# Kernel optimization log

Hardware: AMD Instinct MI355X
Metric: run time of the kernel (lower is better)

Reference implementation:

```python
import jax, jax.numpy as jnp
import numpy as np
from jax import lax

K_SIZE = 5  # dilated_kernel_size


def dcls_kernel(w, p, k=K_SIZE):
    """Build dense (Cout,Cin,k,k) kernel from DCLS v1 bilinear interpolation.
    w: (Cout,Cin,Kc) weights; p: (2,Cout,Cin,Kc) learnable positions."""
    lim = k // 2
    pos = jnp.clip(p, -lim, lim) + lim          # in [0, k-1]
    i = jnp.floor(pos).astype(jnp.int32)
    r = pos - i                                  # bilinear fractions
    Co, Ci, Kc = w.shape
    co = jnp.arange(Co)[:, None, None]
    ci = jnp.arange(Ci)[None, :, None]
    i1, i2 = i[0], i[1]
    r1, r2 = r[0], r[1]
    # scatter into (k+1)x(k+1) grid so i+1 never goes out of bounds, then trim
    K = jnp.zeros((Co, Ci, k + 1, k + 1), w.dtype)
    K = K.at[co, ci, i1,     i2    ].add(w * (1 - r1) * (1 - r2))
    K = K.at[co, ci, i1 + 1, i2    ].add(w * r1 * (1 - r2))
    K = K.at[co, ci, i1,     i2 + 1].add(w * (1 - r1) * r2)
    K = K.at[co, ci, i1 + 1, i2 + 1].add(w * r1 * r2)
    return K[:, :, :k, :k]


def conv2d(x, K, pad):
    return lax.conv_general_dilated(
        x, K, window_strides=(1, 1), padding=[(pad, pad), (pad, pad)],
        dimension_numbers=('NCHW', 'OIHW', 'NCHW'))


def maxpool2(x):
    return lax.reduce_window(x, -jnp.inf, lax.max, (1, 1, 2, 2), (1, 1, 2, 2), 'VALID')


def setup_inputs() -> dict:
    key = jax.random.key(0)
    ks = jax.random.split(key, 12)
    lim = K_SIZE // 2
    B = 4096
    x = jax.random.normal(ks[0], (B, 1, 28, 28), jnp.float32)
    w1 = jax.random.normal(ks[1], (32, 1, 16), jnp.float32) * 0.2
    p1 = jax.random.uniform(ks[2], (2, 32, 1, 16), jnp.float32, -lim, lim)
    b1 = jnp.zeros((32,), jnp.float32)
    w2 = jax.random.normal(ks[3], (64, 32, 32), jnp.float32) * 0.05
    p2 = jax.random.uniform(ks[4], (2, 64, 32, 32), jnp.float32, -lim, lim)
    b2 = jnp.zeros((64,), jnp.float32)
    fc1_w = jax.random.normal(ks[5], (128, 64 * 7 * 7), jnp.float32) * 0.02
    fc1_b = jnp.zeros((128,), jnp.float32)
    fc2_w = jax.random.normal(ks[6], (10, 128), jnp.float32) * 0.08
    fc2_b = jnp.zeros((10,), jnp.float32)
    return dict(x=x, w1=w1, p1=p1, b1=b1, w2=w2, p2=p2, b2=b2,
                fc1_w=fc1_w, fc1_b=fc1_b, fc2_w=fc2_w, fc2_b=fc2_b)


def reference(x, w1, p1, b1, w2, p2, b2, fc1_w, fc1_b, fc2_w, fc2_b):
    h = conv2d(x, dcls_kernel(w1, p1), pad=2) + b1[None, :, None, None]
    h = maxpool2(jax.nn.relu(h))                       # (B,32,14,14)
    h = conv2d(h, dcls_kernel(w2, p2), pad=2) + b2[None, :, None, None]
    h = maxpool2(jax.nn.relu(h))                       # (B,64,7,7)
    h = h.reshape(-1, 64 * 7 * 7)
    h = jax.nn.relu(h @ fc1_w.T + fc1_b)
    return h @ fc2_w.T + fc2_b                         # (B,10)
```

## Files before the change

### kernel.cpp

```cpp
#include <hip/hip_runtime.h>
#include <hip/hip_bf16.h>

typedef __attribute__((ext_vector_type(8))) short short8;
typedef __attribute__((ext_vector_type(4))) short short4v;
typedef __attribute__((ext_vector_type(4))) float float4v;

static __device__ __forceinline__ unsigned short f2bf(float f) {
    unsigned u = __float_as_uint(f);
    unsigned r = (u + 0x7FFF + ((u >> 16) & 1)) >> 16;
    return (unsigned short)r;
}

__global__ __launch_bounds__(256) void prep_all(
    const float* __restrict__ w1, const float* __restrict__ p1,
    const float* __restrict__ w2, const float* __restrict__ p2,
    const float* __restrict__ fc1w,
    unsigned short* __restrict__ K1b,
    unsigned short* __restrict__ Kt,
    unsigned short* __restrict__ w1b) {
    const int blk = blockIdx.x;
    const int t = threadIdx.x;

    if (blk < 8) {
        int cell = blk * 256 + t;
        int co = cell >> 6;
        int k = cell & 63;
        int wr = k >> 3;
        int kx = k & 7;
        float acc = 0.f;
        if (wr < 5 && kx < 5) {
#pragma unroll 8
            for (int kc = 0; kc < 16; ++kc) {
                float wv = w1[co * 16 + kc];
                float pa = p1[co * 16 + kc];
                float pb = p1[512 + co * 16 + kc];
                float pos1 = fminf(fmaxf(pa, -2.f), 2.f) + 2.f;
                float pos2 = fminf(fmaxf(pb, -2.f), 2.f) + 2.f;
                int i1 = (int)floorf(pos1);
                int i2 = (int)floorf(pos2);
                float r1 = pos1 - (float)i1;
                float r2 = pos2 - (float)i2;
                float c = 0.f;
                if (i1 == wr && i2 == kx) c += (1.f - r1) * (1.f - r2);
                if (i1 + 1 == wr && i2 == kx) c += r1 * (1.f - r2);
                if (i1 == wr && i2 + 1 == kx) c += (1.f - r1) * r2;
                if (i1 + 1 == wr && i2 + 1 == kx) c += r1 * r2;
                acc += wv * c;
            }
        }
        K1b[cell] = f2bf(acc);
    } else if (blk < 208) {
        int cell = (blk - 8) * 256 + t;
        int kk = cell >> 11;
        int co = (cell >> 5) & 63;
        int ci = cell & 31;
        int ky = kk / 5;
        int kx = kk - 5 * ky;
        const int base = (co * 32 + ci) * 32;
        float acc = 0.f;
#pragma unroll 8
        for (int kc = 0; kc < 32; ++kc) {
            float wv = w2[base + kc];
            float pa = p2[base + kc];
            float pb = p2[65536 + base + kc];
            float pos1 = fminf(fmaxf(pa, -2.f), 2.f) + 2.f;
            float pos2 = fminf(fmaxf(pb, -2.f), 2.f) + 2.f;
            int i1 = (int)floorf(pos1);
            int i2 = (int)floorf(pos2);
            float r1 = pos1 - (float)i1;
            float r2 = pos2 - (float)i2;
            float c = 0.f;
            if (i1 == ky && i2 == kx) c += (1.f - r1) * (1.f - r2);
            if (i1 + 1 == ky && i2 == kx) c += r1 * (1.f - r2);
            if (i1 == ky && i2 + 1 == kx) c += (1.f - r1) * r2;
            if (i1 + 1 == ky && i2 + 1 == kx) c += r1 * r2;
            acc += wv * c;
        }
        Kt[cell] = f2bf(acc);
    } else {
        int i8 = ((blk - 208) * 256 + t) * 8;
        float4 v0 = *(const float4*)(fc1w + i8);
        float4 v1 = *(const float4*)(fc1w + i8 + 4);
        short8 o = {(short)f2bf(v0.x), (short)f2bf(v0.y), (short)f2bf(v0.z),
                    (short)f2bf(v0.w), (short)f2bf(v1.x), (short)f2bf(v1.y),
                    (short)f2bf(v1.z), (short)f2bf(v1.w)};
        *(short8*)(w1b + i8) = o;
    }
}

__global__ __launch_bounds__(256, 4) void fused_conv_mfma(
    const float* __restrict__ x,
    const unsigned short* __restrict__ K1b,
    const unsigned short* __restrict__ Kt,
    const float* __restrict__ b1,
    const float* __restrict__ b2,
    unsigned short* __restrict__ h2) {
    __shared__ __align__(16) unsigned short h1p[18 * 20 * 40];
    __shared__ __align__(16) unsigned short sm4[4 * 29 * 44];
    __shared__ __align__(16) unsigned short sm_xb[784];

    const int b = blockIdx.x;
    const int tid = threadIdx.x;
    const int lane = tid & 63;
    const int wv = tid >> 6;
    const int n16 = lane & 15;
    const int cig = lane >> 4;

    const int yi = 2 * (n16 >> 3) + ((n16 >> 1) & 1);
    const int xi = 2 * ((n16 >> 2) & 1) + (n16 & 1);
    const int pYo = cig >> 1, pXo = cig & 1;

    for (int t = tid; t < 1800; t += 256) ((uint4*)h1p)[t] = uint4{0, 0, 0, 0};
    {
        const float* xb = x + (size_t)b * 784;
        for (int t = tid; t < 784; t += 256) sm_xb[t] = f2bf(xb[t]);
    }
    __syncthreads();

    if (tid < 116) {
        int s = tid / 29;
        int r = tid - s * 29;
        unsigned short* dst = sm4 + (s * 29 + r) * 44;
        bool rok = r < 28;
#pragma unroll
        for (int g = 0; g < 11; ++g) {
            short4v v;
#pragma unroll
            for (int e = 0; e < 4; ++e) {
                int c = g * 4 + e + s - 4;
                v[e] = (short)((rok && (unsigned)c < 28u) ? sm_xb[r * 28 + c]
                                                          : (unsigned short)0);
            }
            *(short4v*)(dst + g * 4) = v;
        }
    }

    short8 bw[2][2];
    float bias1[2], bias2[4];
#pragma unroll
    for (int cot = 0; cot < 2; ++cot) {
#pragma unroll
        for (int h = 0; h < 2; ++h)
            bw[cot][h] = *(const short8*)(K1b + (cot * 16 + n16) * 64 + h * 32 + cig * 8);
        bias1[cot] = b1[cot * 16 + n16];
    }
#pragma unroll
    for (int cot = 0; cot < 4; ++cot) bias2[cot] = b2[cot * 16 + n16];

    const int s1 = (xi + 2) & 3;
    const int pb1 = (xi + 2) & ~3;
    const unsigned short* a1base = sm4 + s1 * (29 * 44) + pb1;

    __syncthreads();

    for (int i = 0; i < 13; ++i) {
        int t = wv + 4 * i;
        if (t < 49) {
            int tY = t / 7, tX = t - 7 * tY;
            const unsigned short* ab = a1base + 4 * tX;
            int r0 = 4 * tY + yi - 2 + cig;
            int r1 = r0 + 4;
            int rr0 = ((unsigned)r0 < 28u) ? r0 : 28;
            int rr1 = ((unsigned)r1 < 28u) ? r1 : 28;
            short4v lo0 = *(const short4v*)(ab + rr0 * 44);
            short4v hi0 = *(const short4v*)(ab + rr0 * 44 + 4);
            short4v lo1 = *(const short4v*)(ab + rr1 * 44);
            short4v hi1 = *(const short4v*)(ab + rr1 * 44 + 4);
            short8 af0 = {lo0[0], lo0[1], lo0[2], lo0[3], hi0[0], hi0[1], hi0[2], hi0[3]};
            short8 af1 = {lo1[0], lo1[1], lo1[2], lo1[3], hi1[0], hi1[1], hi1[2], hi1[3]};
            int pY = 2 * tY + pYo, pX = 2 * tX + pXo;
#pragma unroll
            for (int cot = 0; cot < 2; ++cot) {
                float4v acc = {0.f, 0.f, 0.f, 0.f};
                acc = __builtin_amdgcn_mfma_f32_16x16x32_bf16(af0, bw[cot][0], acc, 0, 0, 0);
                acc = __builtin_amdgcn_mfma_f32_16x16x32_bf16(af1, bw[cot][1], acc, 0, 0, 0);
                float v = fmaxf(fmaxf(acc[0], acc[1]), fmaxf(acc[2], acc[3]));
                v = fmaxf(v + bias1[cot], 0.f);
                h1p[((pY + 2) * 20 + (pX + 2)) * 40 + cot * 16 + n16] = f2bf(v);
            }
        }
    }
    __syncthreads();

    const unsigned short* Ab[4];
    int pY2[4], pX2[4];
#pragma unroll
    for (int i = 0; i < 4; ++i) {
        int t = wv * 4 + i;
        int tY = t >> 2, tX = t & 3;
        int y2 = 4 * tY + yi;
        y2 = (y2 > 13) ? 13 : y2;
        int x2 = 4 * tX + xi;
        Ab[i] = h1p + (y2 * 20 + x2) * 40 + cig * 8;
        pY2[i] = 2 * tY + pYo;
        pX2[i] = 2 * tX + pXo;
    }

    float4v acc[4][4];
#pragma unroll
    for (int i = 0; i < 4; ++i)
#pragma unroll
        for (int c = 0; c < 4; ++c) acc[i][c] = float4v{0.f, 0.f, 0.f, 0.f};

#pragma unroll
    for (int ky = 0; ky < 5; ++ky) {
#pragma unroll
        for (int kx = 0; kx < 5; ++kx) {
            int kk = ky * 5 + kx;
            short8 wf[4];
#pragma unroll
            for (int cot = 0; cot < 4; ++cot)
                wf[cot] = *(const short8*)(Kt + ((kk * 64 + cot * 16 + n16) * 32 + cig * 8));
#pragma unroll
            for (int i = 0; i < 4; ++i) {
                short8 af = *(const short8*)(Ab[i] + (ky * 20 + kx) * 40);
#pragma unroll
                for (int cot = 0; cot < 4; ++cot)
                    acc[i][cot] = __builtin_amdgcn_mfma_f32_16x16x32_bf16(
                        af, wf[cot], acc[i][cot], 0, 0, 0);
            }
        }
    }

    unsigned short* outb = h2 + (size_t)b * 3136;
#pragma unroll
    for (int i = 0; i < 4; ++i) {
        bool ok = (pY2[i] < 7) & (pX2[i] < 7);
#pragma unroll
        for (int cot = 0; cot < 4; ++cot) {
            float4v a = acc[i][cot];
            float v = fmaxf(fmaxf(a[0], a[1]), fmaxf(a[2], a[3]));
            v = fmaxf(v + bias2[cot], 0.f);
            if (ok)
                outb[(cot * 16 + n16) * 49 + pY2[i] * 7 + pX2[i]] = f2bf(v);
        }
    }
}

__global__ __launch_bounds__(256) void fc1_mfma(
    const unsigned short* __restrict__ A,
    const unsigned short* __restrict__ Wb,
    float* __restrict__ part, size_t PB) {
    __shared__ __align__(16) unsigned short As[64 * 72];
    const int blk = blockIdx.x;
    const int kh = blk % 7;
    const int m0 = (blk / 7) * 64;
    const int tid = threadIdx.x;
    const int wv = tid >> 6;
    const int lane = tid & 63;
    const int n16 = lane & 15;
    const int cig = lane >> 4;

    float4v acc[4][2];
#pragma unroll
    for (int mt = 0; mt < 4; ++mt)
#pragma unroll
        for (int j = 0; j < 2; ++j) acc[mt][j] = float4v{0.f, 0.f, 0.f, 0.f};

    for (int it = 0; it < 7; ++it) {
        int k0 = kh * 448 + it * 64;
        __syncthreads();
#pragma unroll
        for (int i = 0; i < 2; ++i) {
            int p = tid + 256 * i;
            int r = p >> 3, ko = (p & 7) * 8;
            *(short8*)(As + r * 72 + ko) =
                *(const short8*)(A + (size_t)(m0 + r) * 3136 + k0 + ko);
        }
        __syncthreads();
#pragma unroll
        for (int h = 0; h < 2; ++h) {
            short8 af[4];
#pragma unroll
            for (int mt = 0; mt < 4; ++mt)
                af[mt] = *(const short8*)(As + (mt * 16 + n16) * 72 + h * 32 + cig * 8);
            short8 wf[2];
#pragma unroll
            for (int j = 0; j < 2; ++j)
                wf[j] = *(const short8*)(Wb + (size_t)((wv * 2 + j) * 16 + n16) * 3136 +
                                         k0 + h * 32 + cig * 8);
#pragma unroll
            for (int mt = 0; mt < 4; ++mt)
#pragma unroll
                for (int j = 0; j < 2; ++j)
                    acc[mt][j] = __builtin_amdgcn_mfma_f32_16x16x32_bf16(
                        af[mt], wf[j], acc[mt][j], 0, 0, 0);
        }
    }
    float* o = part + (size_t)kh * PB;
#pragma unroll
    for (int mt = 0; mt < 4; ++mt)
#pragma unroll
        for (int j = 0; j < 2; ++j)
#pragma unroll
            for (int r = 0; r < 4; ++r) {
                int row = m0 + mt * 16 + cig * 4 + r;
                o[(size_t)row * 128 + (wv * 2 + j) * 16 + n16] = acc[mt][j][r];
            }
}

__global__ __launch_bounds__(256) void fc2_kernel(
    const float* __restrict__ part, size_t PB,
    const float* __restrict__ fc1b,
    const float* __restrict__ W, const float* __restrict__ bias,
    float* __restrict__ out, int total4) {
    __shared__ float smW[10 * 132];
    __shared__ float smB1[128];
    __shared__ float smB[10];
    int t = threadIdx.x;
    for (int i = t; i < 1280; i += 256) {
        int n = i >> 7, k = i & 127;
        smW[n * 132 + k] = W[i];
    }
    if (t < 128) smB1[t] = fc1b[t];
    if (t < 10) smB[t] = bias[t];
    __syncthreads();
    int idx = blockIdx.x * 256 + t;
    if (idx < total4) {
        int j = idx >> 2;
        int q = idx & 3;
        int b = j / 10;
        int n = j - b * 10;
        const float* pb = part + (size_t)b * 128 + q * 32;
        const float4* bb = (const float4*)(smB1 + q * 32);
        const float4* wr = (const float4*)(smW + n * 132 + q * 32);
        float acc = 0.f;
#pragma unroll
        for (int c = 0; c < 8; ++c) {
            float4 s = *(const float4*)(pb + 4 * c);
#pragma unroll
            for (int jj = 1; jj < 7; ++jj) {
                float4 pj = *(const float4*)(pb + (size_t)jj * PB + 4 * c);
                s.x += pj.x; s.y += pj.y; s.z += pj.z; s.w += pj.w;
            }
            float4 bv = bb[c];
            float4 w = wr[c];
            acc += fmaxf(s.x + bv.x, 0.f) * w.x + fmaxf(s.y + bv.y, 0.f) * w.y +
                   fmaxf(s.z + bv.z, 0.f) * w.z + fmaxf(s.w + bv.w, 0.f) * w.w;
        }
        acc += __shfl_xor(acc, 1);
        acc += __shfl_xor(acc, 2);
        if (q == 0) out[j] = acc + smB[n];
    }
}

extern "C" void kernel_launch(void* const* d_in, const int* in_sizes, int n_in,
                              void* d_out, int out_size, void* d_ws, size_t ws_size,
                              hipStream_t stream) {
    const float* x    = (const float*)d_in[0];
    const float* w1   = (const float*)d_in[1];
    const float* p1   = (const float*)d_in[2];
    const float* b1   = (const float*)d_in[3];
    const float* w2   = (const float*)d_in[4];
    const float* p2   = (const float*)d_in[5];
    const float* b2   = (const float*)d_in[6];
    const float* fc1w = (const float*)d_in[7];
    const float* fc1b = (const float*)d_in[8];
    const float* fc2w = (const float*)d_in[9];
    const float* fc2b = (const float*)d_in[10];
    float* out = (float*)d_out;

    const int B = in_sizes[0] / 784;

    float* ws = (float*)d_ws;
    unsigned short* Kt  = (unsigned short*)ws;
    unsigned short* K1b = (unsigned short*)(ws + 25600);
    unsigned short* w1b = (unsigned short*)(ws + 26624);
    unsigned short* h2b = (unsigned short*)(ws + 227328);
    float* fc1p = ws + 227328 + (size_t)B * 1568;

    prep_all<<<404, 256, 0, stream>>>(w1, p1, w2, p2, fc1w, K1b, Kt, w1b);
    fused_conv_mfma<<<B, 256, 0, stream>>>(x, K1b, Kt, b1, b2, h2b);
    fc1_mfma<<<(B / 64) * 7, 256, 0, stream>>>(h2b, w1b, fc1p, (size_t)B * 128);
    fc2_kernel<<<(B * 10 * 4 + 255) / 256, 256, 0, stream>>>(
        fc1p, (size_t)B * 128, fc1b, fc2w, fc2b, out, B * 10 * 4);
}
```

Measured before the change: 243.4 us.

## Use 32x32x16 MFMA for conv2 and compute all fc2 outputs per row group

The conv2 stage switches from 16x16x32 bf16 MFMA tiles to 32x32x16 tiles, with a new lane-to-pixel mapping and a pooled epilogue taken from the 16-wide accumulator. The goal is fewer MFMA issues and fewer weight fragment loads per output. fc2 is restructured so each 8-lane group handles one batch row and all 10 outputs. The 7 fc1 partial sums are then reduced once per row rather than once per output. The larger accumulators raise register pressure, and the fc2 grid now assumes B is divisible by 32.

```diff
diff --git a/kernel.cpp b/kernel.cpp
--- a/kernel.cpp
+++ b/kernel.cpp
@@ -4,6 +4,7 @@
 typedef __attribute__((ext_vector_type(8))) short short8;
 typedef __attribute__((ext_vector_type(4))) short short4v;
 typedef __attribute__((ext_vector_type(4))) float float4v;
+typedef __attribute__((ext_vector_type(16))) float float16v;
 
 static __device__ __forceinline__ unsigned short f2bf(float f) {
     unsigned u = __float_as_uint(f);
@@ -110,6 +111,12 @@
     const int xi = 2 * ((n16 >> 2) & 1) + (n16 & 1);
     const int pYo = cig >> 1, pXo = cig & 1;
 
+    const int mq = lane & 31;
+    const int Qx = mq >> 2;
+    const int dy2 = (mq >> 1) & 1;
+    const int dx2 = mq & 1;
+    const int hh = lane >> 5;
+
     for (int t = tid; t < 1800; t += 256) ((uint4*)h1p)[t] = uint4{0, 0, 0, 0};
     {
         const float* xb = x + (size_t)b * 784;
@@ -136,7 +143,7 @@
     }
 
     short8 bw[2][2];
-    float bias1[2], bias2[4];
+    float bias1[2], bias2n[2];
 #pragma unroll
     for (int cot = 0; cot < 2; ++cot) {
 #pragma unroll
@@ -145,7 +152,7 @@
         bias1[cot] = b1[cot * 16 + n16];
     }
 #pragma unroll
-    for (int cot = 0; cot < 4; ++cot) bias2[cot] = b2[cot * 16 + n16];
+    for (int nt = 0; nt < 2; ++nt) bias2n[nt] = b2[nt * 32 + mq];
 
     const int s1 = (xi + 2) & 3;
     const int pb1 = (xi + 2) & ~3;
@@ -182,57 +189,72 @@
     }
     __syncthreads();
 
-    const unsigned short* Ab[4];
-    int pY2[4], pX2[4];
-#pragma unroll
-    for (int i = 0; i < 4; ++i) {
-        int t = wv * 4 + i;
-        int tY = t >> 2, tX = t & 3;
-        int y2 = 4 * tY + yi;
-        y2 = (y2 > 13) ? 13 : y2;
-        int x2 = 4 * tX + xi;
-        Ab[i] = h1p + (y2 * 20 + x2) * 40 + cig * 8;
-        pY2[i] = 2 * tY + pYo;
-        pX2[i] = 2 * tX + pXo;
-    }
-
-    float4v acc[4][4];
-#pragma unroll
-    for (int i = 0; i < 4; ++i)
-#pragma unroll
-        for (int c = 0; c < 4; ++c) acc[i][c] = float4v{0.f, 0.f, 0.f, 0.f};
+    int x2 = 2 * Qx + dx2;
+    if (x2 > 13) x2 = 13;
+    int aoff[2][2];
+    int pYv[2];
+#pragma unroll
+    for (int mt = 0; mt < 2; ++mt) {
+        int pY = 2 * wv + mt;
+        int y2 = 2 * pY + dy2;
+        if (y2 > 13) y2 = 13;
+        pYv[mt] = pY;
+#pragma unroll
+        for (int kh2 = 0; kh2 < 2; ++kh2)
+            aoff[mt][kh2] = (y2 * 20 + x2) * 40 + kh2 * 16 + hh * 8;
+    }
+
+    float16v acc2[2][2];
+#pragma unroll
+    for (int mt = 0; mt < 2; ++mt)
+#pragma unroll
+        for (int nt = 0; nt < 2; ++nt)
+#pragma unroll
+            for (int e = 0; e < 16; ++e) acc2[mt][nt][e] = 0.f;
 
 #pragma unroll
     for (int ky = 0; ky < 5; ++ky) {
 #pragma unroll
         for (int kx = 0; kx < 5; ++kx) {
             int kk = ky * 5 + kx;
-            short8 wf[4];
-#pragma unroll
-            for (int cot = 0; cot < 4; ++cot)
-                wf[cot] = *(const short8*)(Kt + ((kk * 64 + cot * 16 + n16) * 32 + cig * 8));
-#pragma unroll
-            for (int i = 0; i < 4; ++i) {
-                short8 af = *(const short8*)(Ab[i] + (ky * 20 + kx) * 40);
-#pragma unroll
-                for (int cot = 0; cot < 4; ++cot)
-                    acc[i][cot] = __builtin_amdgcn_mfma_f32_16x16x32_bf16(
-                        af, wf[cot], acc[i][cot], 0, 0, 0);
+            short8 wf[2][2];
+#pragma unroll
+            for (int nt = 0; nt < 2; ++nt)
+#pragma unroll
+                for (int kh2 = 0; kh2 < 2; ++kh2)
+                    wf[nt][kh2] = *(const short8*)(Kt + kk * 2048 +
+                        (nt * 32 + mq) * 32 + kh2 * 16 + hh * 8);
+#pragma unroll
+            for (int mt = 0; mt < 2; ++mt) {
+                short8 af0 = *(const short8*)(h1p + aoff[mt][0] + (ky * 20 + kx) * 40);
+                short8 af1 = *(const short8*)(h1p + aoff[mt][1] + (ky * 20 + kx) * 40);
+#pragma unroll
+                for (int nt = 0; nt < 2; ++nt) {
+                    acc2[mt][nt] = __builtin_amdgcn_mfma_f32_32x32x16_bf16(
+                        af0, wf[nt][0], acc2[mt][nt], 0, 0, 0);
+                    acc2[mt][nt] = __builtin_amdgcn_mfma_f32_32x32x16_bf16(
+                        af1, wf[nt][1], acc2[mt][nt], 0, 0, 0);
+                }
             }
         }
     }
 
     unsigned short* outb = h2 + (size_t)b * 3136;
 #pragma unroll
-    for (int i = 0; i < 4; ++i) {
-        bool ok = (pY2[i] < 7) & (pX2[i] < 7);
-#pragma unroll
-        for (int cot = 0; cot < 4; ++cot) {
-            float4v a = acc[i][cot];
-            float v = fmaxf(fmaxf(a[0], a[1]), fmaxf(a[2], a[3]));
-            v = fmaxf(v + bias2[cot], 0.f);
-            if (ok)
-                outb[(cot * 16 + n16) * 49 + pY2[i] * 7 + pX2[i]] = f2bf(v);
+    for (int mt = 0; mt < 2; ++mt) {
+        if (pYv[mt] < 7) {
+#pragma unroll
+            for (int nt = 0; nt < 2; ++nt) {
+#pragma unroll
+                for (int g = 0; g < 4; ++g) {
+                    int pX = 2 * g + hh;
+                    float v = fmaxf(fmaxf(acc2[mt][nt][4 * g], acc2[mt][nt][4 * g + 1]),
+                                    fmaxf(acc2[mt][nt][4 * g + 2], acc2[mt][nt][4 * g + 3]));
+                    v = fmaxf(v + bias2n[nt], 0.f);
+                    if (pX < 7)
+                        outb[(nt * 32 + mq) * 49 + pYv[mt] * 7 + pX] = f2bf(v);
+                }
+            }
         }
     }
 }
@@ -303,7 +325,7 @@
     const float* __restrict__ part, size_t PB,
     const float* __restrict__ fc1b,
     const float* __restrict__ W, const float* __restrict__ bias,
-    float* __restrict__ out, int total4) {
+    float* __restrict__ out) {
     __shared__ float smW[10 * 132];
     __shared__ float smB1[128];
     __shared__ float smB[10];
@@ -315,32 +337,48 @@
     if (t < 128) smB1[t] = fc1b[t];
     if (t < 10) smB[t] = bias[t];
     __syncthreads();
-    int idx = blockIdx.x * 256 + t;
-    if (idx < total4) {
-        int j = idx >> 2;
-        int q = idx & 3;
-        int b = j / 10;
-        int n = j - b * 10;
-        const float* pb = part + (size_t)b * 128 + q * 32;
-        const float4* bb = (const float4*)(smB1 + q * 32);
-        const float4* wr = (const float4*)(smW + n * 132 + q * 32);
-        float acc = 0.f;
-#pragma unroll
-        for (int c = 0; c < 8; ++c) {
-            float4 s = *(const float4*)(pb + 4 * c);
-#pragma unroll
-            for (int jj = 1; jj < 7; ++jj) {
-                float4 pj = *(const float4*)(pb + (size_t)jj * PB + 4 * c);
-                s.x += pj.x; s.y += pj.y; s.z += pj.z; s.w += pj.w;
-            }
-            float4 bv = bb[c];
+    const int r = t >> 3;
+    const int q = t & 7;
+    const size_t b = (size_t)blockIdx.x * 32 + r;
+    const float* pb = part + b * 128 + q * 16;
+
+    float rv[16];
+#pragma unroll
+    for (int c = 0; c < 4; ++c) {
+        float4 s = *(const float4*)(pb + 4 * c);
+#pragma unroll
+        for (int j = 1; j < 7; ++j) {
+            float4 pj = *(const float4*)(pb + (size_t)j * PB + 4 * c);
+            s.x += pj.x; s.y += pj.y; s.z += pj.z; s.w += pj.w;
+        }
+        float4 bv = *(const float4*)(smB1 + q * 16 + 4 * c);
+        rv[4 * c + 0] = fmaxf(s.x + bv.x, 0.f);
+        rv[4 * c + 1] = fmaxf(s.y + bv.y, 0.f);
+        rv[4 * c + 2] = fmaxf(s.z + bv.z, 0.f);
+        rv[4 * c + 3] = fmaxf(s.w + bv.w, 0.f);
+    }
+    float acc[10];
+#pragma unroll
+    for (int n = 0; n < 10; ++n) {
+        const float4* wr = (const float4*)(smW + n * 132 + q * 16);
+        float a = 0.f;
+#pragma unroll
+        for (int c = 0; c < 4; ++c) {
             float4 w = wr[c];
-            acc += fmaxf(s.x + bv.x, 0.f) * w.x + fmaxf(s.y + bv.y, 0.f) * w.y +
-                   fmaxf(s.z + bv.z, 0.f) * w.z + fmaxf(s.w + bv.w, 0.f) * w.w;
-        }
-        acc += __shfl_xor(acc, 1);
-        acc += __shfl_xor(acc, 2);
-        if (q == 0) out[j] = acc + smB[n];
+            a += rv[4 * c] * w.x + rv[4 * c + 1] * w.y +
+                 rv[4 * c + 2] * w.z + rv[4 * c + 3] * w.w;
+        }
+        acc[n] = a;
+    }
+#pragma unroll
+    for (int n = 0; n < 10; ++n) {
+        acc[n] += __shfl_xor(acc[n], 1);
+        acc[n] += __shfl_xor(acc[n], 2);
+        acc[n] += __shfl_xor(acc[n], 4);
+    }
+    if (q == 0) {
+#pragma unroll
+        for (int n = 0; n < 10; ++n) out[b * 10 + n] = acc[n] + smB[n];
     }
 }
 
@@ -372,6 +410,6 @@
     prep_all<<<404, 256, 0, stream>>>(w1, p1, w2, p2, fc1w, K1b, Kt, w1b);
     fused_conv_mfma<<<B, 256, 0, stream>>>(x, K1b, Kt, b1, b2, h2b);
     fc1_mfma<<<(B / 64) * 7, 256, 0, stream>>>(h2b, w1b, fc1p, (size_t)B * 128);
-    fc2_kernel<<<(B * 10 * 4 + 255) / 256, 256, 0, stream>>>(
-        fc1p, (size_t)B * 128, fc1b, fc2w, fc2b, out, B * 10 * 4);
-}
+    fc2_kernel<<<B / 32, 256, 0, stream>>>(fc1p, (size_t)B * 128,
+                                           fc1b, fc2w, fc2b, out);
+}
```

Measured after the change: 224.9 us. 1.08x faster.
